# Kernel tuning notes

Hardware: AMD Instinct MI355X
Metric: run time of the kernel (lower is better)

Reference implementation:

```python
import jax, jax.numpy as jnp
import numpy as np

D_MODEL = 1024
N_HEADS = 16
D_K = D_MODEL // N_HEADS
B, S = 2, 2048


def setup_inputs() -> dict:
    key = jax.random.key(0)
    ks = jax.random.split(key, 12)
    scale = 1.0 / np.sqrt(D_MODEL)
    inp = {
        "query": jax.random.normal(ks[0], (B, S, D_MODEL), jnp.float32),
        "key": jax.random.normal(ks[1], (B, S, D_MODEL), jnp.float32),
        "value": jax.random.normal(ks[2], (B, S, D_MODEL), jnp.float32),
        "mask": jnp.tril(jnp.ones((S, S), dtype=bool))[None, None],  # (1,1,S,S) causal
        "W_q": jax.random.normal(ks[3], (D_MODEL, D_MODEL), jnp.float32) * scale,
        "b_q": jnp.zeros((D_MODEL,), jnp.float32),
        "W_k": jax.random.normal(ks[4], (D_MODEL, D_MODEL), jnp.float32) * scale,
        "b_k": jnp.zeros((D_MODEL,), jnp.float32),
        "W_v": jax.random.normal(ks[5], (D_MODEL, D_MODEL), jnp.float32) * scale,
        "b_v": jnp.zeros((D_MODEL,), jnp.float32),
        "W_o": jax.random.normal(ks[6], (D_MODEL, D_MODEL), jnp.float32) * scale,
        "b_o": jnp.zeros((D_MODEL,), jnp.float32),
    }
    return inp


def reference(query, key, value, mask, W_q, b_q, W_k, b_k, W_v, b_v, W_o, b_o):
    b = query.shape[0]
    # Linear projections (torch Linear: x @ W.T + b), split into heads -> (b,h,s,d_k)
    def proj(x, W, bias):
        y = x @ W.T + bias
        return y.reshape(b, -1, N_HEADS, D_K).transpose(0, 2, 1, 3)

    q = proj(query, W_q, b_q)
    k = proj(key, W_k, b_k)
    v = proj(value, W_v, b_v)

    # scores: (b,h,sq,sk)
    scores = jnp.einsum("bhqd,bhkd->bhqk", q, k) / jnp.sqrt(jnp.float32(D_K)).astype(q.dtype)
    scores = jnp.where(mask, scores, jnp.finfo(scores.dtype).min)
    attn = jax.nn.softmax(scores, axis=-1)
    out = jnp.einsum("bhqk,bhkd->bhqd", attn, v)  # (b,h,sq,d_k)
    out = out.transpose(0, 2, 1, 3).reshape(b, -1, D_MODEL)
    return out @ W_o.T + b_o
```

## Files before the change

### kernel.cpp

```cpp
#include <hip/hip_runtime.h>
#include <hip/hip_bf16.h>
#include <stdint.h>

#define D_MODEL 1024
#define NH 16
#define DK 64
#define BB 2
#define SS 2048
#define MROWS (BB*SS)

typedef __attribute__((ext_vector_type(8))) short bf16x8;
typedef __attribute__((ext_vector_type(4))) float f32x4;

__device__ __forceinline__ short to_bf16(float f) {
  __hip_bfloat16 h = __float2bfloat16(f);
  union { __hip_bfloat16 b; short s; } u; u.b = h; return u.s;
}

__device__ __forceinline__ f32x4 mfma16(bf16x8 a, bf16x8 b, f32x4 c) {
  return __builtin_amdgcn_mfma_f32_16x16x32_bf16(a, b, c, 0, 0, 0);
}

__device__ __forceinline__ void gload_lds16(const void* g, void* l) {
  __builtin_amdgcn_global_load_lds(
      (const __attribute__((address_space(1))) unsigned int*)g,
      (__attribute__((address_space(3))) unsigned int*)l,
      16, 0, 0);
}

__device__ __forceinline__ float max3f(float a, float b, float c) {
  return fmaxf(fmaxf(a, b), c);
}

__global__ __launch_bounds__(256) void cvt7(const float* __restrict__ x0,
                                            const float* __restrict__ x1,
                                            const float* __restrict__ x2,
                                            const float* __restrict__ w0,
                                            const float* __restrict__ w1,
                                            const float* __restrict__ w2,
                                            const float* __restrict__ w3,
                                            short* __restrict__ y0,
                                            short* __restrict__ y1,
                                            short* __restrict__ y2,
                                            short* __restrict__ y3,
                                            short* __restrict__ y4,
                                            short* __restrict__ y5,
                                            short* __restrict__ y6) {
  const int z = blockIdx.z;
  const float* x; short* y; int n;
  switch (z) {
    case 0: x = x0; y = y0; n = MROWS * D_MODEL; break;
    case 1: x = x1; y = y1; n = MROWS * D_MODEL; break;
    case 2: x = x2; y = y2; n = MROWS * D_MODEL; break;
    case 3: x = w0; y = y3; n = D_MODEL * D_MODEL; break;
    case 4: x = w1; y = y4; n = D_MODEL * D_MODEL; break;
    case 5: x = w2; y = y5; n = D_MODEL * D_MODEL; break;
    default: x = w3; y = y6; n = D_MODEL * D_MODEL; break;
  }
  const int i = (blockIdx.x * 256 + threadIdx.x) * 4;
  if (i >= n) return;
  const float4 v = *(const float4*)(x + i);
  short4 o;
  o.x = to_bf16(v.x); o.y = to_bf16(v.y); o.z = to_bf16(v.z); o.w = to_bf16(v.w);
  *(short4*)(y + i) = o;
}

__global__ __launch_bounds__(512) void gemm_qkv8(const short* __restrict__ X,
                                                 const short* __restrict__ Wq,
                                                 const short* __restrict__ Wk,
                                                 const short* __restrict__ Wv,
                                                 const float* __restrict__ bq,
                                                 const float* __restrict__ bk,
                                                 const float* __restrict__ bv,
                                                 short* __restrict__ Qh,
                                                 short* __restrict__ Kh,
                                                 short* __restrict__ VT) {
  constexpr int K = 1024, NKT = K / 64;
  __shared__ short Abuf[2][256 * 64];
  __shared__ short Bbuf[2][256 * 64];

  const int tid = threadIdx.x;
  const int w = tid >> 6, lane = tid & 63;
  const int wm = w >> 2, wn = w & 3;
  const int fr = lane & 15, fg = lane >> 4;

  const int m0 = blockIdx.x * 256, n0 = blockIdx.y * 256;
  const int z = m0 >> 12;
  const short* Wt   = z == 0 ? Wq : z == 1 ? Wk : Wv;
  const float* bias = z == 0 ? bq : z == 1 ? bk : bv;

  const int str = tid >> 3;
  const int stc = tid & 7;

  f32x4 acc[8][4] = {};

#define QKV8_STAGE(buf, kt)                                                   \
  do {                                                                        \
    _Pragma("unroll") for (int p = 0; p < 4; ++p) {                           \
      const int row = p * 64 + str;                                           \
      const int cS = stc ^ (row & 7);                                         \
      gload_lds16(X  + (size_t)(m0 + row) * K + (kt) * 64 + cS * 8,           \
                  &Abuf[buf][row * 64 + stc * 8]);                            \
      gload_lds16(Wt + (size_t)(n0 + row) * K + (kt) * 64 + cS * 8,           \
                  &Bbuf[buf][row * 64 + stc * 8]);                            \
    }                                                                         \
  } while (0)

  QKV8_STAGE(0, 0);
  asm volatile("s_waitcnt vmcnt(0)" ::: "memory");
  __syncthreads();

  for (int kt = 0; kt < NKT; ++kt) {
    const int buf = kt & 1;
    if (kt + 1 < NKT) QKV8_STAGE(buf ^ 1, kt + 1);

    const short* Ab = Abuf[buf];
    const short* Bb = Bbuf[buf];
#pragma unroll
    for (int kh = 0; kh < 2; ++kh) {
      const int rchunk = (((kh << 2) + fg) ^ (fr & 7)) << 3;
      bf16x8 bfr[4];
#pragma unroll
      for (int ni = 0; ni < 4; ++ni)
        bfr[ni] = *(const bf16x8*)(Bb + (wn * 64 + ni * 16 + fr) * 64 + rchunk);
#pragma unroll
      for (int mh = 0; mh < 2; ++mh) {
        bf16x8 af[4];
#pragma unroll
        for (int i = 0; i < 4; ++i)
          af[i] = *(const bf16x8*)(Ab + (wm * 128 + (mh * 4 + i) * 16 + fr) * 64 + rchunk);
        __builtin_amdgcn_s_setprio(1);
#pragma unroll
        for (int i = 0; i < 4; ++i)
#pragma unroll
          for (int ni = 0; ni < 4; ++ni)
            acc[mh * 4 + i][ni] = mfma16(af[i], bfr[ni], acc[mh * 4 + i][ni]);
        __builtin_amdgcn_s_setprio(0);
      }
    }
    asm volatile("s_waitcnt vmcnt(0)" ::: "memory");
    __syncthreads();
  }
#undef QKV8_STAGE

  const int zrow0 = m0 & 4095;
  const int b = zrow0 >> 11;
  const int sb = zrow0 & (SS - 1);

  if (z < 2) {
    const float scale = (z == 0) ? 0.18033688011112042f : 1.0f;
    short* dst = (z == 0) ? Qh : Kh;
#pragma unroll
    for (int mi = 0; mi < 8; ++mi)
#pragma unroll
      for (int ni = 0; ni < 4; ++ni) {
        const int col = n0 + wn * 64 + ni * 16 + fr;
        const float bval = bias[col];
        const int h = col >> 6, d = col & 63;
#pragma unroll
        for (int r = 0; r < 4; ++r) {
          const int s = sb + wm * 128 + mi * 16 + fg * 4 + r;
          dst[((size_t)(b * NH + h) * SS + s) * DK + d] =
              to_bf16((acc[mi][ni][r] + bval) * scale);
        }
      }
  } else {
#pragma unroll
    for (int mi = 0; mi < 8; ++mi)
#pragma unroll
      for (int ni = 0; ni < 4; ++ni) {
        const int col = n0 + wn * 64 + ni * 16 + fr;
        const float bval = bias[col];
        const int h = col >> 6, d = col & 63;
        const int s0 = sb + wm * 128 + mi * 16 + fg * 4;
        short4 sv = {to_bf16(acc[mi][ni][0] + bval), to_bf16(acc[mi][ni][1] + bval),
                     to_bf16(acc[mi][ni][2] + bval), to_bf16(acc[mi][ni][3] + bval)};
        *(short4*)(VT + ((size_t)(b * NH + h) * DK + d) * SS + s0) = sv;
      }
  }
}

__global__ __launch_bounds__(256) void gemm_out(const short* __restrict__ A,
                                                const short* __restrict__ Wt,
                                                const float* __restrict__ bias,
                                                float* __restrict__ Y) {
  constexpr int K = 1024, NSTEP = K / 32;
  __shared__ __align__(16) char pool[36864];
  const int tid = threadIdx.x;
  const int w = tid >> 6, lane = tid & 63;
  const int m0 = blockIdx.x * 128, n0 = blockIdx.y * 64;
  const int wm = w >> 1, wn = w & 1;
  const int fr = lane & 15, fg = lane >> 4;
  const int srow = tid >> 2;
  const int scolS = ((tid & 3) ^ ((srow >> 1) & 3)) * 8;
  const int scolD = (tid & 3) * 8;
  const int fcs = (fg ^ ((fr >> 1) & 3)) * 8;

  f32x4 acc[4][2] = {};

#define OUT_STAGE(buf, k0)                                                    \
  do {                                                                        \
    short* As_ = (short*)(pool + (buf) * 12288);                              \
    short* Bs_ = (short*)(pool + (buf) * 12288 + 8192);                       \
    _Pragma("unroll") for (int i = 0; i < 2; ++i) {                           \
      const int row = i * 64 + srow;                                          \
      gload_lds16(A + (size_t)(m0 + row) * K + (k0) + scolS,                  \
                  As_ + row * 32 + scolD);                                    \
    }                                                                         \
    gload_lds16(Wt + (size_t)(n0 + srow) * K + (k0) + scolS,                  \
                Bs_ + srow * 32 + scolD);                                     \
  } while (0)

  OUT_STAGE(0, 0);
  OUT_STAGE(1, 32);
  asm volatile("s_waitcnt vmcnt(3)" ::: "memory");
  __syncthreads();

  for (int t = 0; t < NSTEP; ++t) {
    if (t + 2 < NSTEP) OUT_STAGE((t + 2) % 3, (t + 2) * 32);

    const short* Ab = (const short*)(pool + (t % 3) * 12288);
    const short* Bb = (const short*)(pool + (t % 3) * 12288 + 8192);
    bf16x8 af[4], bfr[2];
#pragma unroll
    for (int i = 0; i < 4; ++i)
      af[i] = *(const bf16x8*)(Ab + (wm * 64 + i * 16 + fr) * 32 + fcs);
#pragma unroll
    for (int i = 0; i < 2; ++i)
      bfr[i] = *(const bf16x8*)(Bb + (wn * 32 + i * 16 + fr) * 32 + fcs);
    __builtin_amdgcn_s_setprio(1);
#pragma unroll
    for (int mi = 0; mi < 4; ++mi)
#pragma unroll
      for (int ni = 0; ni < 2; ++ni)
        acc[mi][ni] = mfma16(af[mi], bfr[ni], acc[mi][ni]);
    __builtin_amdgcn_s_setprio(0);

    if (t + 2 < NSTEP)
      asm volatile("s_waitcnt vmcnt(3)" ::: "memory");
    else
      asm volatile("s_waitcnt vmcnt(0)" ::: "memory");
    __syncthreads();
  }
#undef OUT_STAGE

#pragma unroll
  for (int mi = 0; mi < 4; ++mi)
#pragma unroll
    for (int ni = 0; ni < 2; ++ni) {
      const int col = n0 + wn * 32 + ni * 16 + fr;
      const float bval = bias[col];
#pragma unroll
      for (int r = 0; r < 4; ++r) {
        const int row = m0 + wm * 64 + mi * 16 + fg * 4 + r;
        Y[(size_t)row * D_MODEL + col] = acc[mi][ni][r] + bval;
      }
    }
}

__global__ __launch_bounds__(256) void attn_kernel(const short* __restrict__ Qh,
                                                   const short* __restrict__ Kh,
                                                   const short* __restrict__ VT,
                                                   short* __restrict__ AO) {
  __shared__ short Ks[2][2][64 * 64];
  __shared__ short Vs[2][2][64 * 64];
  __shared__ short P_lds[4][16 * 64];

  const int tid = threadIdx.x, w = tid >> 6, lane = tid & 63;
  const int fr = lane & 15, fg = lane >> 4;
  const int kr = fg * 4;
  const int swz = (fr & 7) << 4;

  const int bid = blockIdx.x;
  const int lid = ((bid & 7) << 6) | (bid >> 3);
  const int bh = lid >> 4;
  const int j = lid & 15;
  const int b = bh >> 4, h = bh & 15;

  const short* Qp = Qh + (size_t)bh * SS * DK;
  const short* Kp = Kh + (size_t)bh * SS * DK;
  const short* Vp = VT + (size_t)bh * DK * SS;

  const int sc_c = tid & 7;
  const int sc_r = tid >> 3;

  const int T0 = (j + 2) >> 1;
  const int koff0 = j * 64 - (T0 - 1) * 128;
  const int koff1 = (31 - j) * 64 - (16 - T0) * 128;

  bf16x8 qf[2];
#pragma unroll
  for (int hh = 0; hh < 2; ++hh)
    qf[hh] = *(const bf16x8*)(Qp + (size_t)(j * 64 + w * 16 + fr) * DK + hh * 32 + fg * 8);

  const short onev = (fr == 0) ? (short)0x3F80 : (short)0;
  const bf16x8 af4 = {onev, onev, onev, onev, onev, onev, onev, onev};

  f32x4 o[5] = {};
  float m_run = -1e30f;
  f32x4 stA[8], stB[8];

#define KK0(g) ((((g) < T0) ? (g) : ((g) - T0)) * 128)
#define STAGE_K(buf, kk0)                                                     \
  do {                                                                        \
    _Pragma("unroll") for (int hf = 0; hf < 2; ++hf)                          \
    _Pragma("unroll") for (int p = 0; p < 2; ++p) {                           \
      const int row = p * 32 + sc_r;                                          \
      const int sc = sc_c ^ (row & 7);                                        \
      gload_lds16(Kp + (size_t)((kk0) + hf * 64 + row) * DK + sc * 8,         \
                  &Ks[buf][hf][row * 64 + sc_c * 8]);                         \
    }                                                                         \
  } while (0)
#define STAGE_V(buf, kk0)                                                     \
  do {                                                                        \
    _Pragma("unroll") for (int hf = 0; hf < 2; ++hf)                          \
    _Pragma("unroll") for (int p = 0; p < 2; ++p) {                           \
      const int row = p * 32 + sc_r;                                          \
      const int sc = sc_c ^ (row & 7);                                        \
      gload_lds16(Vp + (size_t)row * SS + (kk0) + hf * 64 + sc * 8,           \
                  &Vs[buf][hf][row * 64 + sc_c * 8]);                         \
    }                                                                         \
  } while (0)

#define SOFTMAX_PV(ST, bufPrev)                                               \
  do {                                                                        \
    float mm[8];                                                              \
    _Pragma("unroll") for (int i = 0; i < 8; ++i)                             \
      mm[i] = fmaxf(fmaxf(ST[i][0], ST[i][1]), fmaxf(ST[i][2], ST[i][3]));    \
    float pmax = fmaxf(max3f(mm[0], mm[1], mm[2]),                            \
                       fmaxf(max3f(mm[3], mm[4], mm[5]), fmaxf(mm[6], mm[7]))); \
    pmax = fmaxf(pmax, __shfl_xor(pmax, 16));                                 \
    pmax = fmaxf(pmax, __shfl_xor(pmax, 32));                                 \
    if (!__all(pmax <= m_run + 11.0f)) {                                      \
      const float mn = fmaxf(m_run, pmax);                                    \
      const float al = __builtin_amdgcn_exp2f(m_run - mn);                    \
      m_run = mn;                                                             \
      _Pragma("unroll") for (int t = 0; t < 5; ++t)                           \
        _Pragma("unroll") for (int r = 0; r < 4; ++r) o[t][r] *= al;          \
    }                                                                         \
    _Pragma("unroll") for (int hf = 0; hf < 2; ++hf) {                        \
      char* base = (char*)P_lds[w];                                           \
      _Pragma("unroll") for (int kt = 0; kt < 4; ++kt) {                      \
        short4 sv;                                                            \
        sv.x = to_bf16(__builtin_amdgcn_exp2f(ST[hf * 4 + kt][0] - m_run));   \
        sv.y = to_bf16(__builtin_amdgcn_exp2f(ST[hf * 4 + kt][1] - m_run));   \
        sv.z = to_bf16(__builtin_amdgcn_exp2f(ST[hf * 4 + kt][2] - m_run));   \
        sv.w = to_bf16(__builtin_amdgcn_exp2f(ST[hf * 4 + kt][3] - m_run));   \
        *(short4*)(base + ((fr * 128 + kt * 32 + fg * 8) ^ swz)) = sv;        \
      }                                                                       \
      asm volatile("s_waitcnt lgkmcnt(0)" ::: "memory");                      \
      const char* VsB = (const char*)Vs[bufPrev][hf];                         \
      __builtin_amdgcn_s_setprio(1);                                          \
      _Pragma("unroll") for (int c = 0; c < 2; ++c) {                         \
        const bf16x8 pf = *(const bf16x8*)((const char*)P_lds[w] +            \
                                           ((fr * 128 + c * 64 + fg * 16) ^ swz)); \
        _Pragma("unroll") for (int t = 0; t < 4; ++t) {                       \
          const bf16x8 vfb = *(const bf16x8*)(VsB + (t * 16 + fr) * 128 +     \
                                              ((c * 64 + fg * 16) ^ swz));    \
          o[t] = mfma16(vfb, pf, o[t]);                                       \
        }                                                                     \
        o[4] = mfma16(af4, pf, o[4]);                                         \
      }                                                                       \
      __builtin_amdgcn_s_setprio(0);                                          \
    }                                                                         \
  } while (0)

#define STEP(CUR, PREV, g)                                                    \
  do {                                                                        \
    if ((g) == T0) {                                                          \
      _Pragma("unroll") for (int hh = 0; hh < 2; ++hh)                        \
        qf[hh] = *(const bf16x8*)(Qp + (size_t)((31 - j) * 64 + w * 16 + fr) * DK + hh * 32 + fg * 8); \
    }                                                                         \
    if ((g) + 1 < 17) STAGE_K(((g) + 1) & 1, KK0((g) + 1));                   \
    {                                                                         \
      __builtin_amdgcn_s_setprio(1);                                          \
      _Pragma("unroll") for (int hf = 0; hf < 2; ++hf) {                      \
        const char* KsB = (const char*)Ks[(g) & 1][hf];                       \
        _Pragma("unroll") for (int kt = 0; kt < 4; ++kt) {                    \
          const bf16x8 k0f = *(const bf16x8*)(KsB + (kt * 16 + fr) * 128 + ((fg * 16) ^ swz)); \
          const bf16x8 k1f = *(const bf16x8*)(KsB + (kt * 16 + fr) * 128 + ((64 + fg * 16) ^ swz)); \
          f32x4 zz = {};                                                      \
          zz = mfma16(k0f, qf[0], zz);                                        \
          zz = mfma16(k1f, qf[1], zz);                                        \
          CUR[hf * 4 + kt] = zz;                                              \
        }                                                                     \
      }                                                                       \
      __builtin_amdgcn_s_setprio(0);                                          \
    }                                                                         \
    if ((g) == T0 - 1 || (g) == 16) {                                         \
      const int koff = ((g) == 16) ? koff1 : koff0;                           \
      _Pragma("unroll") for (int hf = 0; hf < 2; ++hf)                        \
        _Pragma("unroll") for (int kt = 0; kt < 4; ++kt)                      \
          _Pragma("unroll") for (int r = 0; r < 4; ++r)                       \
            if (hf * 64 + kt * 16 + kr + r > koff + w * 16 + fr)              \
              CUR[hf * 4 + kt][r] = -1e30f;                                   \
    }                                                                         \
    if ((g) > 0) {                                                            \
      SOFTMAX_PV(PREV, ((g) - 1) & 1);                                        \
      if ((g) == T0) {                                                        \
        store_o(j * 64);                                                      \
        _Pragma("unroll") for (int t = 0; t < 5; ++t)                         \
          _Pragma("unroll") for (int r = 0; r < 4; ++r) o[t][r] = 0.f;        \
        m_run = -1e30f;                                                       \
      }                                                                       \
    }                                                                         \
    __syncthreads();                                                          \
    if ((g) + 1 < 17) {                                                       \
      STAGE_V(((g) + 1) & 1, KK0((g) + 1));                                   \
      asm volatile("s_waitcnt vmcnt(4)" ::: "memory");                        \
    } else {                                                                  \
      asm volatile("s_waitcnt vmcnt(0)" ::: "memory");                        \
    }                                                                         \
  } while (0)

  auto store_o = [&](int qbase) {
    const float l = __shfl(o[4][0], fr);
    const float inv = 1.0f / l;
    const int s = qbase + w * 16 + fr;
#pragma unroll
    for (int t = 0; t < 4; ++t) {
      short4 ov = {to_bf16(o[t][0] * inv), to_bf16(o[t][1] * inv),
                   to_bf16(o[t][2] * inv), to_bf16(o[t][3] * inv)};
      *(short4*)(AO + (size_t)(b * SS + s) * D_MODEL + h * 64 + t * 16 + kr) = ov;
    }
  };

  STAGE_K(0, 0);
  STAGE_V(0, 0);
  asm volatile("s_waitcnt vmcnt(0)" ::: "memory");
  __syncthreads();

  for (int gg = 0; gg < 16; gg += 2) {
    STEP(stA, stB, gg);
    STEP(stB, stA, gg + 1);
  }
  STEP(stA, stB, 16);

  SOFTMAX_PV(stA, 0);
  store_o((31 - j) * 64);
#undef STEP
#undef SOFTMAX_PV
#undef STAGE_K
#undef STAGE_V
#undef KK0
}

extern "C" void kernel_launch(void* const* d_in, const int* in_sizes, int n_in,
                              void* d_out, int out_size, void* d_ws, size_t ws_size,
                              hipStream_t stream) {
  const float* q  = (const float*)d_in[0];
  const float* k  = (const float*)d_in[1];
  const float* v  = (const float*)d_in[2];
  const float* Wq = (const float*)d_in[4];
  const float* bq = (const float*)d_in[5];
  const float* Wk = (const float*)d_in[6];
  const float* bk = (const float*)d_in[7];
  const float* Wv = (const float*)d_in[8];
  const float* bv = (const float*)d_in[9];
  const float* Wo = (const float*)d_in[10];
  const float* bo = (const float*)d_in[11];

  char* ws = (char*)d_ws;
  const size_t MB = 1u << 20;
  short* Xq = (short*)(ws + 0 * MB);
  short* Xk = (short*)(ws + 8 * MB);
  short* Xv = (short*)(ws + 16 * MB);
  short* Bq = (short*)(ws + 24 * MB);
  short* Bk = (short*)(ws + 26 * MB);
  short* Bv = (short*)(ws + 28 * MB);
  short* Bo = (short*)(ws + 30 * MB);
  short* Qh = (short*)(ws + 32 * MB);
  short* Kh = (short*)(ws + 40 * MB);
  short* VT = (short*)(ws + 48 * MB);
  short* AO = (short*)(ws + 56 * MB);

  cvt7<<<dim3(MROWS * D_MODEL / 1024, 1, 7), 256, 0, stream>>>(
      q, k, v, Wq, Wk, Wv, Wo, Xq, Xk, Xv, Bq, Bk, Bv, Bo);

  gemm_qkv8<<<dim3(3 * MROWS / 256, D_MODEL / 256), 512, 0, stream>>>(
      Xq, Bq, Bk, Bv, bq, bk, bv, Qh, Kh, VT);

  attn_kernel<<<dim3(512), 256, 0, stream>>>(Qh, Kh, VT, AO);

  gemm_out<<<dim3(MROWS / 128, D_MODEL / 64), 256, 0, stream>>>(AO, Bo, bo, (float*)d_out);
}
```

Measured before the change: 117.5 us.

## Split attention into one query tile per block with single-buffered LDS

The attention kernel stops pairing two complementary causal query tiles per block and launches 1024 blocks, each handling one 64-row query tile. Blocks are ordered so that long and short tiles interleave, to balance load across compute units. The double-buffered K/V LDS staging is replaced by single buffers, and launch bounds request 4 blocks per CU, aiming at higher occupancy to hide latency. In exchange the software pipeline that overlapped the QK product with V staging and softmax is lost, since each iteration now waits on its loads between two barriers.

```diff
diff --git a/kernel.cpp b/kernel.cpp
--- a/kernel.cpp
+++ b/kernel.cpp
@@ -258,12 +258,12 @@
     }
 }
 
-__global__ __launch_bounds__(256) void attn_kernel(const short* __restrict__ Qh,
-                                                   const short* __restrict__ Kh,
-                                                   const short* __restrict__ VT,
-                                                   short* __restrict__ AO) {
-  __shared__ short Ks[2][2][64 * 64];
-  __shared__ short Vs[2][2][64 * 64];
+__global__ __launch_bounds__(256, 4) void attn_kernel(const short* __restrict__ Qh,
+                                                      const short* __restrict__ Kh,
+                                                      const short* __restrict__ VT,
+                                                      short* __restrict__ AO) {
+  __shared__ short Ks[128 * 64];
+  __shared__ short Vs[64 * 128];
   __shared__ short P_lds[4][16 * 64];
 
   const int tid = threadIdx.x, w = tid >> 6, lane = tid & 63;
@@ -272,177 +272,155 @@
   const int swz = (fr & 7) << 4;
 
   const int bid = blockIdx.x;
-  const int lid = ((bid & 7) << 6) | (bid >> 3);
-  const int bh = lid >> 4;
-  const int j = lid & 15;
+  const int lid = ((bid & 7) << 7) | (bid >> 3);
+  const int bh = lid >> 5;
+  const int i5 = lid & 31;
+  const int O = (i5 & 1) ? (i5 >> 1) : (31 - (i5 >> 1));
+  const int s = (bh & 1) ? (31 - O) : O;
   const int b = bh >> 4, h = bh & 15;
+  const int qb = s * 64;
+  const int T = (s + 2) >> 1;
+  const int koff = (s & 1) ? 64 : 0;
 
   const short* Qp = Qh + (size_t)bh * SS * DK;
   const short* Kp = Kh + (size_t)bh * SS * DK;
   const short* Vp = VT + (size_t)bh * DK * SS;
 
-  const int sc_c = tid & 7;
-  const int sc_r = tid >> 3;
-
-  const int T0 = (j + 2) >> 1;
-  const int koff0 = j * 64 - (T0 - 1) * 128;
-  const int koff1 = (31 - j) * 64 - (16 - T0) * 128;
+  const int kst_r = tid >> 3, kst_c = tid & 7;
+  const int vst_r = tid >> 4, vst_c = tid & 15;
 
   bf16x8 qf[2];
 #pragma unroll
   for (int hh = 0; hh < 2; ++hh)
-    qf[hh] = *(const bf16x8*)(Qp + (size_t)(j * 64 + w * 16 + fr) * DK + hh * 32 + fg * 8);
+    qf[hh] = *(const bf16x8*)(Qp + (size_t)(qb + w * 16 + fr) * DK + hh * 32 + fg * 8);
 
   const short onev = (fr == 0) ? (short)0x3F80 : (short)0;
   const bf16x8 af4 = {onev, onev, onev, onev, onev, onev, onev, onev};
 
   f32x4 o[5] = {};
   float m_run = -1e30f;
-  f32x4 stA[8], stB[8];
-
-#define KK0(g) ((((g) < T0) ? (g) : ((g) - T0)) * 128)
-#define STAGE_K(buf, kk0)                                                     \
+  f32x4 st[8];
+
+#define STAGE_K(kk0)                                                          \
   do {                                                                        \
-    _Pragma("unroll") for (int hf = 0; hf < 2; ++hf)                          \
-    _Pragma("unroll") for (int p = 0; p < 2; ++p) {                           \
-      const int row = p * 32 + sc_r;                                          \
-      const int sc = sc_c ^ (row & 7);                                        \
-      gload_lds16(Kp + (size_t)((kk0) + hf * 64 + row) * DK + sc * 8,         \
-                  &Ks[buf][hf][row * 64 + sc_c * 8]);                         \
+    _Pragma("unroll") for (int p = 0; p < 4; ++p) {                           \
+      const int row = p * 32 + kst_r;                                         \
+      const int sc = kst_c ^ (row & 7);                                       \
+      gload_lds16(Kp + (size_t)((kk0) + row) * DK + sc * 8,                   \
+                  Ks + row * 64 + kst_c * 8);                                 \
     }                                                                         \
   } while (0)
-#define STAGE_V(buf, kk0)                                                     \
+#define STAGE_V(kk0)                                                          \
   do {                                                                        \
-    _Pragma("unroll") for (int hf = 0; hf < 2; ++hf)                          \
-    _Pragma("unroll") for (int p = 0; p < 2; ++p) {                           \
-      const int row = p * 32 + sc_r;                                          \
-      const int sc = sc_c ^ (row & 7);                                        \
-      gload_lds16(Vp + (size_t)row * SS + (kk0) + hf * 64 + sc * 8,           \
-                  &Vs[buf][hf][row * 64 + sc_c * 8]);                         \
+    _Pragma("unroll") for (int p = 0; p < 4; ++p) {                           \
+      const int row = p * 16 + vst_r;                                         \
+      const int sc = vst_c ^ (row & 7);                                       \
+      gload_lds16(Vp + (size_t)row * SS + (kk0) + sc * 8,                     \
+                  Vs + row * 128 + vst_c * 8);                                \
     }                                                                         \
   } while (0)
 
-#define SOFTMAX_PV(ST, bufPrev)                                               \
-  do {                                                                        \
-    float mm[8];                                                              \
-    _Pragma("unroll") for (int i = 0; i < 8; ++i)                             \
-      mm[i] = fmaxf(fmaxf(ST[i][0], ST[i][1]), fmaxf(ST[i][2], ST[i][3]));    \
-    float pmax = fmaxf(max3f(mm[0], mm[1], mm[2]),                            \
-                       fmaxf(max3f(mm[3], mm[4], mm[5]), fmaxf(mm[6], mm[7]))); \
-    pmax = fmaxf(pmax, __shfl_xor(pmax, 16));                                 \
-    pmax = fmaxf(pmax, __shfl_xor(pmax, 32));                                 \
-    if (!__all(pmax <= m_run + 11.0f)) {                                      \
-      const float mn = fmaxf(m_run, pmax);                                    \
-      const float al = __builtin_amdgcn_exp2f(m_run - mn);                    \
-      m_run = mn;                                                             \
-      _Pragma("unroll") for (int t = 0; t < 5; ++t)                           \
-        _Pragma("unroll") for (int r = 0; r < 4; ++r) o[t][r] *= al;          \
-    }                                                                         \
-    _Pragma("unroll") for (int hf = 0; hf < 2; ++hf) {                        \
-      char* base = (char*)P_lds[w];                                           \
-      _Pragma("unroll") for (int kt = 0; kt < 4; ++kt) {                      \
-        short4 sv;                                                            \
-        sv.x = to_bf16(__builtin_amdgcn_exp2f(ST[hf * 4 + kt][0] - m_run));   \
-        sv.y = to_bf16(__builtin_amdgcn_exp2f(ST[hf * 4 + kt][1] - m_run));   \
-        sv.z = to_bf16(__builtin_amdgcn_exp2f(ST[hf * 4 + kt][2] - m_run));   \
-        sv.w = to_bf16(__builtin_amdgcn_exp2f(ST[hf * 4 + kt][3] - m_run));   \
-        *(short4*)(base + ((fr * 128 + kt * 32 + fg * 8) ^ swz)) = sv;        \
-      }                                                                       \
-      asm volatile("s_waitcnt lgkmcnt(0)" ::: "memory");                      \
-      const char* VsB = (const char*)Vs[bufPrev][hf];                         \
-      __builtin_amdgcn_s_setprio(1);                                          \
-      _Pragma("unroll") for (int c = 0; c < 2; ++c) {                         \
-        const bf16x8 pf = *(const bf16x8*)((const char*)P_lds[w] +            \
-                                           ((fr * 128 + c * 64 + fg * 16) ^ swz)); \
-        _Pragma("unroll") for (int t = 0; t < 4; ++t) {                       \
-          const bf16x8 vfb = *(const bf16x8*)(VsB + (t * 16 + fr) * 128 +     \
-                                              ((c * 64 + fg * 16) ^ swz));    \
-          o[t] = mfma16(vfb, pf, o[t]);                                       \
-        }                                                                     \
-        o[4] = mfma16(af4, pf, o[4]);                                         \
-      }                                                                       \
-      __builtin_amdgcn_s_setprio(0);                                          \
-    }                                                                         \
-  } while (0)
-
-#define STEP(CUR, PREV, g)                                                    \
-  do {                                                                        \
-    if ((g) == T0) {                                                          \
-      _Pragma("unroll") for (int hh = 0; hh < 2; ++hh)                        \
-        qf[hh] = *(const bf16x8*)(Qp + (size_t)((31 - j) * 64 + w * 16 + fr) * DK + hh * 32 + fg * 8); \
-    }                                                                         \
-    if ((g) + 1 < 17) STAGE_K(((g) + 1) & 1, KK0((g) + 1));                   \
-    {                                                                         \
-      __builtin_amdgcn_s_setprio(1);                                          \
-      _Pragma("unroll") for (int hf = 0; hf < 2; ++hf) {                      \
-        const char* KsB = (const char*)Ks[(g) & 1][hf];                       \
-        _Pragma("unroll") for (int kt = 0; kt < 4; ++kt) {                    \
-          const bf16x8 k0f = *(const bf16x8*)(KsB + (kt * 16 + fr) * 128 + ((fg * 16) ^ swz)); \
-          const bf16x8 k1f = *(const bf16x8*)(KsB + (kt * 16 + fr) * 128 + ((64 + fg * 16) ^ swz)); \
-          f32x4 zz = {};                                                      \
-          zz = mfma16(k0f, qf[0], zz);                                        \
-          zz = mfma16(k1f, qf[1], zz);                                        \
-          CUR[hf * 4 + kt] = zz;                                              \
-        }                                                                     \
-      }                                                                       \
-      __builtin_amdgcn_s_setprio(0);                                          \
-    }                                                                         \
-    if ((g) == T0 - 1 || (g) == 16) {                                         \
-      const int koff = ((g) == 16) ? koff1 : koff0;                           \
-      _Pragma("unroll") for (int hf = 0; hf < 2; ++hf)                        \
-        _Pragma("unroll") for (int kt = 0; kt < 4; ++kt)                      \
-          _Pragma("unroll") for (int r = 0; r < 4; ++r)                       \
-            if (hf * 64 + kt * 16 + kr + r > koff + w * 16 + fr)              \
-              CUR[hf * 4 + kt][r] = -1e30f;                                   \
-    }                                                                         \
-    if ((g) > 0) {                                                            \
-      SOFTMAX_PV(PREV, ((g) - 1) & 1);                                        \
-      if ((g) == T0) {                                                        \
-        store_o(j * 64);                                                      \
-        _Pragma("unroll") for (int t = 0; t < 5; ++t)                         \
-          _Pragma("unroll") for (int r = 0; r < 4; ++r) o[t][r] = 0.f;        \
-        m_run = -1e30f;                                                       \
-      }                                                                       \
-    }                                                                         \
-    __syncthreads();                                                          \
-    if ((g) + 1 < 17) {                                                       \
-      STAGE_V(((g) + 1) & 1, KK0((g) + 1));                                   \
-      asm volatile("s_waitcnt vmcnt(4)" ::: "memory");                        \
-    } else {                                                                  \
-      asm volatile("s_waitcnt vmcnt(0)" ::: "memory");                        \
-    }                                                                         \
-  } while (0)
-
-  auto store_o = [&](int qbase) {
-    const float l = __shfl(o[4][0], fr);
-    const float inv = 1.0f / l;
-    const int s = qbase + w * 16 + fr;
-#pragma unroll
-    for (int t = 0; t < 4; ++t) {
-      short4 ov = {to_bf16(o[t][0] * inv), to_bf16(o[t][1] * inv),
-                   to_bf16(o[t][2] * inv), to_bf16(o[t][3] * inv)};
-      *(short4*)(AO + (size_t)(b * SS + s) * D_MODEL + h * 64 + t * 16 + kr) = ov;
+  auto softmax_pv = [&]() {
+    float mm[8];
+#pragma unroll
+    for (int i = 0; i < 8; ++i)
+      mm[i] = fmaxf(fmaxf(st[i][0], st[i][1]), fmaxf(st[i][2], st[i][3]));
+    float pmax = fmaxf(max3f(mm[0], mm[1], mm[2]),
+                       fmaxf(max3f(mm[3], mm[4], mm[5]), fmaxf(mm[6], mm[7])));
+    pmax = fmaxf(pmax, __shfl_xor(pmax, 16));
+    pmax = fmaxf(pmax, __shfl_xor(pmax, 32));
+
+    if (!__all(pmax <= m_run + 11.0f)) {
+      const float mn = fmaxf(m_run, pmax);
+      const float al = __builtin_amdgcn_exp2f(m_run - mn);
+      m_run = mn;
+#pragma unroll
+      for (int t = 0; t < 5; ++t)
+#pragma unroll
+        for (int r = 0; r < 4; ++r) o[t][r] *= al;
+    }
+
+#pragma unroll
+    for (int hf = 0; hf < 2; ++hf) {
+      char* base = (char*)P_lds[w];
+#pragma unroll
+      for (int kt = 0; kt < 4; ++kt) {
+        const int kk = hf * 4 + kt;
+        short4 sv;
+        sv.x = to_bf16(__builtin_amdgcn_exp2f(st[kk][0] - m_run));
+        sv.y = to_bf16(__builtin_amdgcn_exp2f(st[kk][1] - m_run));
+        sv.z = to_bf16(__builtin_amdgcn_exp2f(st[kk][2] - m_run));
+        sv.w = to_bf16(__builtin_amdgcn_exp2f(st[kk][3] - m_run));
+        *(short4*)(base + ((fr * 128 + kt * 32 + fg * 8) ^ swz)) = sv;
+      }
+      asm volatile("s_waitcnt lgkmcnt(0)" ::: "memory");
+
+      const char* VsB = (const char*)Vs;
+      __builtin_amdgcn_s_setprio(1);
+#pragma unroll
+      for (int c = 0; c < 2; ++c) {
+        const bf16x8 pf = *(const bf16x8*)((const char*)P_lds[w] +
+                                           ((fr * 128 + c * 64 + fg * 16) ^ swz));
+#pragma unroll
+        for (int t = 0; t < 4; ++t) {
+          const bf16x8 vfb = *(const bf16x8*)(VsB + (t * 16 + fr) * 256 +
+                                              ((hf * 128 + c * 64 + fg * 16) ^ swz));
+          o[t] = mfma16(vfb, pf, o[t]);
+        }
+        o[4] = mfma16(af4, pf, o[4]);
+      }
+      __builtin_amdgcn_s_setprio(0);
     }
   };
 
-  STAGE_K(0, 0);
-  STAGE_V(0, 0);
+  STAGE_K(0);
   asm volatile("s_waitcnt vmcnt(0)" ::: "memory");
   __syncthreads();
 
-  for (int gg = 0; gg < 16; gg += 2) {
-    STEP(stA, stB, gg);
-    STEP(stB, stA, gg + 1);
-  }
-  STEP(stA, stB, 16);
-
-  SOFTMAX_PV(stA, 0);
-  store_o((31 - j) * 64);
-#undef STEP
-#undef SOFTMAX_PV
+  for (int g = 0; g < T; ++g) {
+    if (g > 0) softmax_pv();
+
+    {
+      const char* KsB = (const char*)Ks;
+      __builtin_amdgcn_s_setprio(1);
+#pragma unroll
+      for (int kt = 0; kt < 8; ++kt) {
+        const bf16x8 k0f = *(const bf16x8*)(KsB + (kt * 16 + fr) * 128 + ((fg * 16) ^ swz));
+        const bf16x8 k1f = *(const bf16x8*)(KsB + (kt * 16 + fr) * 128 + ((64 + fg * 16) ^ swz));
+        f32x4 zz = {};
+        zz = mfma16(k0f, qf[0], zz);
+        zz = mfma16(k1f, qf[1], zz);
+        st[kt] = zz;
+      }
+      __builtin_amdgcn_s_setprio(0);
+    }
+    if (g == T - 1) {
+#pragma unroll
+      for (int kt = 0; kt < 8; ++kt)
+#pragma unroll
+        for (int r = 0; r < 4; ++r)
+          if (kt * 16 + kr + r > koff + w * 16 + fr) st[kt][r] = -1e30f;
+    }
+
+    __syncthreads();
+    STAGE_V(g * 128);
+    if (g + 1 < T) STAGE_K((g + 1) * 128);
+    asm volatile("s_waitcnt vmcnt(0)" ::: "memory");
+    __syncthreads();
+  }
+
+  softmax_pv();
+  const float l = __shfl(o[4][0], fr);
+  const float inv = 1.0f / l;
+  const int sq = qb + w * 16 + fr;
+#pragma unroll
+  for (int t = 0; t < 4; ++t) {
+    short4 ov = {to_bf16(o[t][0] * inv), to_bf16(o[t][1] * inv),
+                 to_bf16(o[t][2] * inv), to_bf16(o[t][3] * inv)};
+    *(short4*)(AO + (size_t)(b * SS + sq) * D_MODEL + h * 64 + t * 16 + kr) = ov;
+  }
 #undef STAGE_K
 #undef STAGE_V
-#undef KK0
 }
 
 extern "C" void kernel_launch(void* const* d_in, const int* in_sizes, int n_in,
@@ -480,7 +458,7 @@
   gemm_qkv8<<<dim3(3 * MROWS / 256, D_MODEL / 256), 512, 0, stream>>>(
       Xq, Bq, Bk, Bv, bq, bk, bv, Qh, Kh, VT);
 
-  attn_kernel<<<dim3(512), 256, 0, stream>>>(Qh, Kh, VT, AO);
+  attn_kernel<<<dim3(1024), 256, 0, stream>>>(Qh, Kh, VT, AO);
 
   gemm_out<<<dim3(MROWS / 128, D_MODEL / 64), 256, 0, stream>>>(AO, Bo, bo, (float*)d_out);
 }
```

New measurement: 120.0 us. +2.1%, slower.
